# Kernel tuning notes

Hardware: AMD Instinct MI355X
Metric: run time of the kernel (lower is better)

The kernel has to match this reference:

```python
import jax, jax.numpy as jnp
import numpy as np

EMBED = 1024
HEADS = 16
HEAD_DIM = EMBED // HEADS
MAX_REL = 8
B, S = 4, 1024


def setup_inputs() -> dict:
    key = jax.random.key(0)
    ks = jax.random.split(key, 12)
    lim = 1.0 / np.sqrt(EMBED)
    def lin(k):
        k1, k2 = jax.random.split(k)
        W = jax.random.uniform(k1, (EMBED, EMBED), jnp.float32, -lim, lim)
        b = jax.random.uniform(k2, (EMBED,), jnp.float32, -lim, lim)
        return W, b
    Wq, bq = lin(ks[0]); Wk, bk = lin(ks[1]); Wv, bv = lin(ks[2]); Wo, bo = lin(ks[3])
    return {
        'query': jax.random.normal(ks[4], (B, S, EMBED), jnp.float32),
        'key': jax.random.normal(ks[5], (B, S, EMBED), jnp.float32),
        'value': jax.random.normal(ks[6], (B, S, EMBED), jnp.float32),
        'mask': jnp.zeros((B, S, S), dtype=bool),
        'Wq': Wq, 'bq': bq, 'Wk': Wk, 'bk': bk, 'Wv': Wv, 'bv': bv,
        'Wo': Wo, 'bo': bo,
        'rel_bias': jnp.zeros((HEADS, 2 * MAX_REL + 1), jnp.float32),
    }


def _split_heads(x):
    b, s, _ = x.shape
    return x.reshape(b, s, HEADS, HEAD_DIM).transpose(0, 2, 1, 3)  # [b,h,s,d]


def reference(query, key, value, mask, Wq, bq, Wk, bk, Wv, bv, Wo, bo, rel_bias):
    scale = jnp.sqrt(jnp.float32(HEAD_DIM))
    Q = _split_heads(query @ Wq.T + bq)
    K = _split_heads(key @ Wk.T + bk)
    V = _split_heads(value @ Wv.T + bv)
    scores = jnp.einsum('bhqd,bhkd->bhqk', Q, K) / scale
    # relative position bias: rel_bias[h, clip(j-i)+max]
    idx = jnp.arange(query.shape[1])
    rel = jnp.clip(idx[None, :] - idx[:, None], -MAX_REL, MAX_REL) + MAX_REL  # [s,s]
    bias = rel_bias[:, rel]  # [h,s,s]
    scores = scores + bias[None]
    scores = jnp.where(mask[:, None, :, :], -jnp.inf, scores)
    attn = jax.nn.softmax(scores, axis=-1)
    ctx = jnp.einsum('bhqk,bhkd->bhqd', attn, V)
    b, h, s, d = ctx.shape
    out = ctx.transpose(0, 2, 1, 3).reshape(b, s, h * d) @ Wo.T + bo
    return out, attn, scores
```

## Files before the change

kernel.cpp:

```cpp
#include <hip/hip_runtime.h>

typedef __bf16 bf16_t;
typedef bf16_t bf16x4 __attribute__((ext_vector_type(4)));
typedef bf16_t bf16x8 __attribute__((ext_vector_type(8)));
typedef float f32x4 __attribute__((ext_vector_type(4)));
typedef float f32x8 __attribute__((ext_vector_type(8)));

#define B_N 4
#define S_N 1024
#define E_N 1024
#define H_N 16
#define D_N 64

#define MFMA16 __builtin_amdgcn_mfma_f32_16x16x32_bf16

static __device__ __forceinline__ bf16_t f2b(float x) { return (bf16_t)x; }

static __device__ __forceinline__ void gload_lds16(const void* g, void* l) {
  __builtin_amdgcn_global_load_lds(
      (const __attribute__((address_space(1))) unsigned int*)g,
      (__attribute__((address_space(3))) unsigned int*)l, 16, 0, 0);
}

static __device__ __forceinline__ void lds_barrier() {
  asm volatile("s_waitcnt lgkmcnt(0)\n\ts_barrier" ::: "memory");
  __builtin_amdgcn_sched_barrier(0);
}

__global__ __launch_bounds__(256) void convert_kernel(
    const float* __restrict__ q, const float* __restrict__ k, const float* __restrict__ v,
    const float* __restrict__ wq, const float* __restrict__ wk,
    const float* __restrict__ wv, const float* __restrict__ wo,
    bf16_t* __restrict__ dq, bf16_t* __restrict__ dk, bf16_t* __restrict__ dv,
    bf16_t* __restrict__ dwq, bf16_t* __restrict__ dwk,
    bf16_t* __restrict__ dwv, bf16_t* __restrict__ dwo)
{
  const size_t e = ((size_t)blockIdx.x * 256 + threadIdx.x) * 8;
  const float* src; bf16_t* dst; size_t off;
  if (e < 12582912ull) {
    const int which = (int)(e >> 22);
    off = e & 4194303ull;
    src = which == 0 ? q : (which == 1 ? k : v);
    dst = which == 0 ? dq : (which == 1 ? dk : dv);
  } else {
    const size_t e2 = e - 12582912ull;
    const int which = (int)(e2 >> 20);
    off = e2 & 1048575ull;
    src = which == 0 ? wq : (which == 1 ? wk : (which == 2 ? wv : wo));
    dst = which == 0 ? dwq : (which == 1 ? dwk : (which == 2 ? dwv : dwo));
  }
  f32x8 x = *(const f32x8*)(src + off);
  bf16x8 r;
#pragma unroll
  for (int i = 0; i < 8; ++i) r[i] = f2b(x[i]);
  *(bf16x8*)(dst + off) = r;
}

__global__ __launch_bounds__(256) void mask_rowany(
    const unsigned char* __restrict__ mask, unsigned char* __restrict__ flags)
{
  const int row = blockIdx.x * 4 + (threadIdx.x >> 6);
  const int lane = threadIdx.x & 63;
  const uint4 v = *(const uint4*)(mask + (size_t)row * 1024 + lane * 16);
  const unsigned int any = v.x | v.y | v.z | v.w;
  const unsigned long long bal = __ballot(any != 0);
  if (lane == 0) flags[row] = bal ? 1 : 0;
}

__global__ __launch_bounds__(256) void qkv_gemm(
    const bf16_t* __restrict__ qA, const bf16_t* __restrict__ kA, const bf16_t* __restrict__ vA,
    const bf16_t* __restrict__ Wq, const bf16_t* __restrict__ Wk, const bf16_t* __restrict__ Wv,
    const float* __restrict__ bq, const float* __restrict__ bk, const float* __restrict__ bv,
    bf16_t* __restrict__ Qo, bf16_t* __restrict__ Ko, bf16_t* __restrict__ Vto)
{
  const int z = blockIdx.z;
  const bf16_t* A = z == 0 ? qA : (z == 1 ? kA : vA);
  const bf16_t* W = z == 0 ? Wq : (z == 1 ? Wk : Wv);
  const float* bias = z == 0 ? bq : (z == 1 ? bk : bv);

  __shared__ bf16_t As[128 * 32];
  __shared__ bf16_t Bs[128 * 32];
  const int tid = threadIdx.x;
  const int m0 = blockIdx.y * 128, n0 = blockIdx.x * 128;
  const int lane = tid & 63, wid = tid >> 6;
  const int wr = wid >> 1, wc = wid & 1;
  const int lr = lane & 15, lh = lane >> 4;
  const int sr = lane >> 2, sc = (lane & 3) * 8;
  f32x4 acc[4][4] = {};
  for (int k0 = 0; k0 < 1024; k0 += 32) {
#pragma unroll
    for (int i = 0; i < 2; ++i) {
      const int br = wid * 32 + i * 16;
      gload_lds16(&A[(size_t)(m0 + br + sr) * 1024 + k0 + sc], &As[br * 32]);
      gload_lds16(&W[(size_t)(n0 + br + sr) * 1024 + k0 + sc], &Bs[br * 32]);
    }
    __syncthreads();
    bf16x8 af[4], bw[4];
#pragma unroll
    for (int m = 0; m < 4; ++m)
      af[m] = *(const bf16x8*)&As[(wr * 64 + m * 16 + lr) * 32 + lh * 8];
#pragma unroll
    for (int n = 0; n < 4; ++n)
      bw[n] = *(const bf16x8*)&Bs[(wc * 64 + n * 16 + lr) * 32 + lh * 8];
#pragma unroll
    for (int m = 0; m < 4; ++m)
#pragma unroll
      for (int n = 0; n < 4; ++n)
        acc[m][n] = MFMA16(af[m], bw[n], acc[m][n], 0, 0, 0);
    __syncthreads();
  }
#pragma unroll
  for (int n = 0; n < 4; ++n) {
    const int col = n0 + wc * 64 + n * 16 + lr;
    const float bv_ = bias[col];
    const int h = col >> 6, d = col & 63;
#pragma unroll
    for (int m = 0; m < 4; ++m) {
      const int row0 = m0 + wr * 64 + m * 16 + lh * 4;
#pragma unroll
      for (int r = 0; r < 4; ++r) {
        const int row = row0 + r;
        const float v = acc[m][n][r] + bv_;
        const int b = row >> 10, s = row & 1023;
        if (z == 0)
          Qo[((size_t)(b * H_N + h) * S_N + s) * D_N + d] = f2b(v);
        else if (z == 1)
          Ko[((size_t)(b * H_N + h) * S_N + s) * D_N + d] = f2b(v);
        else
          Vto[((size_t)(b * H_N + h) * D_N + d) * S_N + s] = f2b(v);
      }
    }
  }
}

__global__ __launch_bounds__(256) void out_gemm(
    const bf16_t* __restrict__ A, const bf16_t* __restrict__ W,
    const float* __restrict__ bias, float* __restrict__ Co)
{
  __shared__ bf16_t As[128 * 32];
  __shared__ bf16_t Bs[128 * 32];
  const int tid = threadIdx.x;
  const int m0 = blockIdx.y * 128, n0 = blockIdx.x * 128;
  const int lane = tid & 63, wid = tid >> 6;
  const int wr = wid >> 1, wc = wid & 1;
  const int lr = lane & 15, lh = lane >> 4;
  const int sr = lane >> 2, sc = (lane & 3) * 8;
  f32x4 acc[4][4] = {};
  for (int k0 = 0; k0 < 1024; k0 += 32) {
#pragma unroll
    for (int i = 0; i < 2; ++i) {
      const int br = wid * 32 + i * 16;
      gload_lds16(&A[(size_t)(m0 + br + sr) * 1024 + k0 + sc], &As[br * 32]);
      gload_lds16(&W[(size_t)(n0 + br + sr) * 1024 + k0 + sc], &Bs[br * 32]);
    }
    __syncthreads();
    bf16x8 af[4], bw[4];
#pragma unroll
    for (int m = 0; m < 4; ++m)
      af[m] = *(const bf16x8*)&As[(wr * 64 + m * 16 + lr) * 32 + lh * 8];
#pragma unroll
    for (int n = 0; n < 4; ++n)
      bw[n] = *(const bf16x8*)&Bs[(wc * 64 + n * 16 + lr) * 32 + lh * 8];
#pragma unroll
    for (int m = 0; m < 4; ++m)
#pragma unroll
      for (int n = 0; n < 4; ++n)
        acc[m][n] = MFMA16(af[m], bw[n], acc[m][n], 0, 0, 0);
    __syncthreads();
  }
#pragma unroll
  for (int n = 0; n < 4; ++n) {
    const int col = n0 + wc * 64 + n * 16 + lr;
    const float bv_ = bias[col];
#pragma unroll
    for (int m = 0; m < 4; ++m) {
      const int row0 = m0 + wr * 64 + m * 16 + lh * 4;
#pragma unroll
      for (int r = 0; r < 4; ++r)
        Co[(size_t)(row0 + r) * E_N + col] = acc[m][n][r] + bv_;
    }
  }
}

static __device__ __forceinline__ f32x4 score4(
    f32x4 acc, int qrow, int kc, const unsigned char* __restrict__ mrow,
    const float* __restrict__ rbh, float rb_lo, float rb_hi, bool um)
{
  const int d0 = kc - qrow;
  float b0, b1, b2, b3;
  if (d0 >= 8) { b0 = b1 = b2 = b3 = rb_hi; }
  else if (d0 <= -11) { b0 = b1 = b2 = b3 = rb_lo; }
  else {
    int dd;
    dd = d0;     dd = dd < -8 ? -8 : (dd > 8 ? 8 : dd); b0 = rbh[dd + 8];
    dd = d0 + 1; dd = dd < -8 ? -8 : (dd > 8 ? 8 : dd); b1 = rbh[dd + 8];
    dd = d0 + 2; dd = dd < -8 ? -8 : (dd > 8 ? 8 : dd); b2 = rbh[dd + 8];
    dd = d0 + 3; dd = dd < -8 ? -8 : (dd > 8 ? 8 : dd); b3 = rbh[dd + 8];
  }
  f32x4 s;
  s[0] = acc[0] * 0.125f + b0;
  s[1] = acc[1] * 0.125f + b1;
  s[2] = acc[2] * 0.125f + b2;
  s[3] = acc[3] * 0.125f + b3;
  if (um) {
    const unsigned int mw = *(const unsigned int*)(mrow + kc);
    const float NEG = -__builtin_inff();
    if (mw & 0xffu)       s[0] = NEG;
    if (mw & 0xff00u)     s[1] = NEG;
    if (mw & 0xff0000u)   s[2] = NEG;
    if (mw & 0xff000000u) s[3] = NEG;
  }
  return s;
}

__global__ __launch_bounds__(256) void fused_attn(
    const bf16_t* __restrict__ Q, const bf16_t* __restrict__ K,
    const bf16_t* __restrict__ Vt,
    const unsigned char* __restrict__ mask, const unsigned char* __restrict__ rowflag,
    const float* __restrict__ rel_bias,
    float* __restrict__ scores, float* __restrict__ attn, bf16_t* __restrict__ ctx)
{
  __shared__ bf16_t Ktile[64 * 64];
  __shared__ bf16_t Vtile[64 * 64];
  __shared__ float S_lds[4][16][68];

  const int bh = blockIdx.y, b = bh >> 4, h = bh & 15;
  const int q0 = blockIdx.x * 64;
  const int tid = threadIdx.x;
  const int w = tid >> 6, lane = tid & 63;
  const int lr = lane & 15, lh = lane >> 4;
  const int qrow = q0 + w * 16 + lr;

  const bf16_t* Qh = Q + (size_t)bh * (S_N * D_N);
  const bf16_t* Kh = K + (size_t)bh * (S_N * D_N);
  const bf16_t* Vh = Vt + (size_t)bh * (D_N * S_N);
  const unsigned char* mrow = mask + (size_t)b * S_N * S_N + (size_t)qrow * S_N;
  float* Sbase = scores + (size_t)bh * S_N * S_N + (size_t)(q0 + w * 16) * S_N;
  float* Abase = attn + (size_t)bh * S_N * S_N + (size_t)(q0 + w * 16) * S_N;
  const float* rbh = rel_bias + h * 17;
  const float rb_lo = rbh[0], rb_hi = rbh[16];
  const float NEG = -__builtin_inff();
  const float THR = 8.0f;
  const bool um = rowflag[b * S_N + qrow] != 0;

  const int sg_row0 = tid >> 3, sg_c = tid & 7;
  const int sg_row1 = (tid + 256) >> 3;
  const int sg_s0 = (sg_c ^ (sg_row0 & 7)) * 8;
  const int sg_s1 = (sg_c ^ (sg_row1 & 7)) * 8;

  bf16x8 qa0 = *(const bf16x8*)&Qh[(size_t)qrow * D_N + lh * 8];
  bf16x8 qa1 = *(const bf16x8*)&Qh[(size_t)qrow * D_N + 32 + lh * 8];

  const int ks0 = (lh ^ (lr & 7)) * 8;
  const int ks1 = ((4 + lh) ^ (lr & 7)) * 8;

  float mrun = NEG, srun = 0.f;
  for (int kt = 0; kt < 16; ++kt) {
    const int kb = kt * 64;
    lds_barrier();
    *(bf16x8*)&Ktile[sg_row0 * 64 + sg_s0] =
        *(const bf16x8*)&Kh[(size_t)(kb + sg_row0) * D_N + sg_c * 8];
    *(bf16x8*)&Ktile[sg_row1 * 64 + sg_s1] =
        *(const bf16x8*)&Kh[(size_t)(kb + sg_row1) * D_N + sg_c * 8];
    lds_barrier();
    f32x4 sr4[4];
    float mloc = NEG;
#pragma unroll
    for (int t = 0; t < 4; ++t) {
      const int krow = t * 16 + lr;
      bf16x8 ka0 = *(const bf16x8*)&Ktile[krow * 64 + ks0];
      bf16x8 ka1 = *(const bf16x8*)&Ktile[krow * 64 + ks1];
      f32x4 acc = {};
      acc = MFMA16(ka0, qa0, acc, 0, 0, 0);
      acc = MFMA16(ka1, qa1, acc, 0, 0, 0);
      const int kc = kb + t * 16 + 4 * lh;
      f32x4 s = score4(acc, qrow, kc, mrow, rbh, rb_lo, rb_hi, um);
      sr4[t] = s;
      *(f32x4*)&S_lds[w][lr][t * 16 + 4 * lh] = s;
      mloc = fmaxf(mloc, fmaxf(fmaxf(s[0], s[1]), fmaxf(s[2], s[3])));
    }
    mloc = fmaxf(mloc, __shfl_xor(mloc, 16));
    mloc = fmaxf(mloc, __shfl_xor(mloc, 32));
    if (__any(mloc - mrun > THR)) {
      const float mn = fmaxf(mrun, mloc);
      if (mn > NEG) {
        srun = srun * __expf(mrun - mn);
        mrun = mn;
      }
    }
    const bool live = mrun > NEG;
    float ls = 0.f;
#pragma unroll
    for (int t = 0; t < 4; ++t) {
      f32x4 s = sr4[t];
      float e0 = live ? __expf(s[0] - mrun) : 0.f;
      float e1 = live ? __expf(s[1] - mrun) : 0.f;
      float e2 = live ? __expf(s[2] - mrun) : 0.f;
      float e3 = live ? __expf(s[3] - mrun) : 0.f;
      ls += (e0 + e1) + (e2 + e3);
    }
    srun += ls;
#pragma unroll
    for (int i = 0; i < 4; ++i) {
      const int row = 4 * i + lh;
      f32x4 sv = *(const f32x4*)&S_lds[w][row][lr * 4];
      __builtin_nontemporal_store(sv, (f32x4*)&Sbase[(size_t)row * S_N + kb + lr * 4]);
    }
  }
  srun += __shfl_xor(srun, 16);
  srun += __shfl_xor(srun, 32);
  const float M = mrun;
  const float invs = 1.0f / srun;

  f32x4 accp[4] = {};
  for (int kt = 0; kt < 16; ++kt) {
    const int kb = kt * 64;
    lds_barrier();
    *(bf16x8*)&Ktile[sg_row0 * 64 + sg_s0] =
        *(const bf16x8*)&Kh[(size_t)(kb + sg_row0) * D_N + sg_c * 8];
    *(bf16x8*)&Ktile[sg_row1 * 64 + sg_s1] =
        *(const bf16x8*)&Kh[(size_t)(kb + sg_row1) * D_N + sg_c * 8];
    *(bf16x8*)&Vtile[sg_row0 * 64 + sg_s0] =
        *(const bf16x8*)&Vh[(size_t)sg_row0 * S_N + kb + sg_c * 8];
    *(bf16x8*)&Vtile[sg_row1 * 64 + sg_s1] =
        *(const bf16x8*)&Vh[(size_t)sg_row1 * S_N + kb + sg_c * 8];
    lds_barrier();
#pragma unroll
    for (int t = 0; t < 4; ++t) {
      const int krow = t * 16 + lr;
      bf16x8 ka0 = *(const bf16x8*)&Ktile[krow * 64 + ks0];
      bf16x8 ka1 = *(const bf16x8*)&Ktile[krow * 64 + ks1];
      f32x4 acc = {};
      acc = MFMA16(ka0, qa0, acc, 0, 0, 0);
      acc = MFMA16(ka1, qa1, acc, 0, 0, 0);
      const int kc = kb + t * 16 + 4 * lh;
      f32x4 s = score4(acc, qrow, kc, mrow, rbh, rb_lo, rb_hi, um);
      f32x4 p;
#pragma unroll
      for (int j = 0; j < 4; ++j) p[j] = __expf(s[j] - M) * invs;
      *(f32x4*)&S_lds[w][lr][t * 16 + 4 * lh] = p;
    }
#pragma unroll
    for (int i = 0; i < 4; ++i) {
      const int row = 4 * i + lh;
      f32x4 pv = *(const f32x4*)&S_lds[w][row][lr * 4];
      __builtin_nontemporal_store(pv, (f32x4*)&Abase[(size_t)row * S_N + kb + lr * 4]);
    }
#pragma unroll
    for (int ch = 0; ch < 2; ++ch) {
      f32x8 pf = *(const f32x8*)&S_lds[w][lr][ch * 32 + lh * 8];
      bf16x8 pa;
#pragma unroll
      for (int j = 0; j < 8; ++j) pa[j] = f2b(pf[j]);
#pragma unroll
      for (int dt = 0; dt < 4; ++dt) {
        const int drow = dt * 16 + lr;
        bf16x8 vb = *(const bf16x8*)&Vtile[drow * 64 + (((ch * 4 + lh) ^ (lr & 7)) * 8)];
        accp[dt] = MFMA16(pa, vb, accp[dt], 0, 0, 0);
      }
    }
  }
#pragma unroll
  for (int dt = 0; dt < 4; ++dt)
#pragma unroll
    for (int r = 0; r < 4; ++r)
      ctx[((size_t)(b * S_N + q0 + w * 16 + 4 * lh + r)) * E_N + h * 64 + dt * 16 + lr] =
          f2b(accp[dt][r]);
}

extern "C" void kernel_launch(void* const* d_in, const int* in_sizes, int n_in,
                              void* d_out, int out_size, void* d_ws, size_t ws_size,
                              hipStream_t stream) {
  (void)in_sizes; (void)n_in; (void)out_size; (void)ws_size;
  const float* query = (const float*)d_in[0];
  const float* key   = (const float*)d_in[1];
  const float* value = (const float*)d_in[2];
  const unsigned char* mask = (const unsigned char*)d_in[3];
  const float* Wq = (const float*)d_in[4];
  const float* bq = (const float*)d_in[5];
  const float* Wk = (const float*)d_in[6];
  const float* bk = (const float*)d_in[7];
  const float* Wv = (const float*)d_in[8];
  const float* bv = (const float*)d_in[9];
  const float* Wo = (const float*)d_in[10];
  const float* bo = (const float*)d_in[11];
  const float* rel_bias = (const float*)d_in[12];

  float* out_f    = (float*)d_out;
  float* attn_f   = out_f + (size_t)4194304;
  float* scores_f = attn_f + (size_t)67108864;

  char* ws = (char*)d_ws;
  bf16_t* qbf  = (bf16_t*)(ws);
  bf16_t* kbf  = (bf16_t*)(ws + (8ull  << 20));
  bf16_t* vbf  = (bf16_t*)(ws + (16ull << 20));
  bf16_t* Wqb  = (bf16_t*)(ws + (24ull << 20));
  bf16_t* Wkb  = (bf16_t*)(ws + (26ull << 20));
  bf16_t* Wvb  = (bf16_t*)(ws + (28ull << 20));
  bf16_t* Wob  = (bf16_t*)(ws + (30ull << 20));
  bf16_t* Qbf  = (bf16_t*)(ws + (32ull << 20));
  bf16_t* Kbf  = (bf16_t*)(ws + (40ull << 20));
  bf16_t* Vtbf = (bf16_t*)(ws + (48ull << 20));
  bf16_t* CTX  = (bf16_t*)(ws + (56ull << 20));
  unsigned char* FLAGS = (unsigned char*)(ws + (64ull << 20));

  convert_kernel<<<dim3(8192), dim3(256), 0, stream>>>(
      query, key, value, Wq, Wk, Wv, Wo, qbf, kbf, vbf, Wqb, Wkb, Wvb, Wob);
  mask_rowany<<<dim3(1024), dim3(256), 0, stream>>>(mask, FLAGS);
  qkv_gemm<<<dim3(8, 32, 3), dim3(256), 0, stream>>>(
      qbf, kbf, vbf, Wqb, Wkb, Wvb, bq, bk, bv, Qbf, Kbf, Vtbf);
  fused_attn<<<dim3(16, 64), dim3(256), 0, stream>>>(
      Qbf, Kbf, Vtbf, mask, FLAGS, rel_bias, scores_f, attn_f, CTX);
  out_gemm<<<dim3(8, 32), dim3(256), 0, stream>>>(CTX, Wob, bo, out_f);
}
```

Baseline: 223.0 us.

## Merge mask scan into convert, shrink out_gemm tiles, prefetch K/V tiles in attention

Folds the mask row-any kernel into the conversion kernel as extra blocks, removing one launch. The output GEMM tile shrinks from 128x128 to 64x128, doubling the grid from 256 to 512 blocks so more CUs are busy, at the cost of less operand reuse per block. In the fused attention kernel, K and V tiles for the next iteration are loaded into registers while the current tile is in use, to hide global load latency. This raises register pressure.

```diff
diff --git a/kernel.cpp b/kernel.cpp
--- a/kernel.cpp
+++ b/kernel.cpp
@@ -27,14 +27,24 @@
   __builtin_amdgcn_sched_barrier(0);
 }
 
-__global__ __launch_bounds__(256) void convert_kernel(
+__global__ __launch_bounds__(256) void convert_mask_kernel(
     const float* __restrict__ q, const float* __restrict__ k, const float* __restrict__ v,
     const float* __restrict__ wq, const float* __restrict__ wk,
     const float* __restrict__ wv, const float* __restrict__ wo,
     bf16_t* __restrict__ dq, bf16_t* __restrict__ dk, bf16_t* __restrict__ dv,
     bf16_t* __restrict__ dwq, bf16_t* __restrict__ dwk,
-    bf16_t* __restrict__ dwv, bf16_t* __restrict__ dwo)
+    bf16_t* __restrict__ dwv, bf16_t* __restrict__ dwo,
+    const unsigned char* __restrict__ mask, unsigned char* __restrict__ flags)
 {
+  if (blockIdx.x >= 8192) {
+    const int row = (blockIdx.x - 8192) * 4 + (threadIdx.x >> 6);
+    const int lane = threadIdx.x & 63;
+    const uint4 mv = *(const uint4*)(mask + (size_t)row * 1024 + lane * 16);
+    const unsigned int any = mv.x | mv.y | mv.z | mv.w;
+    const unsigned long long bal = __ballot(any != 0);
+    if (lane == 0) flags[row] = bal ? 1 : 0;
+    return;
+  }
   const size_t e = ((size_t)blockIdx.x * 256 + threadIdx.x) * 8;
   const float* src; bf16_t* dst; size_t off;
   if (e < 12582912ull) {
@@ -56,17 +66,6 @@
   *(bf16x8*)(dst + off) = r;
 }
 
-__global__ __launch_bounds__(256) void mask_rowany(
-    const unsigned char* __restrict__ mask, unsigned char* __restrict__ flags)
-{
-  const int row = blockIdx.x * 4 + (threadIdx.x >> 6);
-  const int lane = threadIdx.x & 63;
-  const uint4 v = *(const uint4*)(mask + (size_t)row * 1024 + lane * 16);
-  const unsigned int any = v.x | v.y | v.z | v.w;
-  const unsigned long long bal = __ballot(any != 0);
-  if (lane == 0) flags[row] = bal ? 1 : 0;
-}
-
 __global__ __launch_bounds__(256) void qkv_gemm(
     const bf16_t* __restrict__ qA, const bf16_t* __restrict__ kA, const bf16_t* __restrict__ vA,
     const bf16_t* __restrict__ Wq, const bf16_t* __restrict__ Wk, const bf16_t* __restrict__ Wv,
@@ -137,44 +136,43 @@
     const bf16_t* __restrict__ A, const bf16_t* __restrict__ W,
     const float* __restrict__ bias, float* __restrict__ Co)
 {
-  __shared__ bf16_t As[128 * 32];
+  __shared__ bf16_t As[64 * 32];
   __shared__ bf16_t Bs[128 * 32];
   const int tid = threadIdx.x;
-  const int m0 = blockIdx.y * 128, n0 = blockIdx.x * 128;
+  const int m0 = blockIdx.y * 64, n0 = blockIdx.x * 128;
   const int lane = tid & 63, wid = tid >> 6;
-  const int wr = wid >> 1, wc = wid & 1;
   const int lr = lane & 15, lh = lane >> 4;
   const int sr = lane >> 2, sc = (lane & 3) * 8;
-  f32x4 acc[4][4] = {};
+  f32x4 acc[4][2] = {};
   for (int k0 = 0; k0 < 1024; k0 += 32) {
+    gload_lds16(&A[(size_t)(m0 + wid * 16 + sr) * 1024 + k0 + sc], &As[wid * 16 * 32]);
 #pragma unroll
     for (int i = 0; i < 2; ++i) {
       const int br = wid * 32 + i * 16;
-      gload_lds16(&A[(size_t)(m0 + br + sr) * 1024 + k0 + sc], &As[br * 32]);
       gload_lds16(&W[(size_t)(n0 + br + sr) * 1024 + k0 + sc], &Bs[br * 32]);
     }
     __syncthreads();
-    bf16x8 af[4], bw[4];
+    bf16x8 af[4], bw[2];
 #pragma unroll
     for (int m = 0; m < 4; ++m)
-      af[m] = *(const bf16x8*)&As[(wr * 64 + m * 16 + lr) * 32 + lh * 8];
-#pragma unroll
-    for (int n = 0; n < 4; ++n)
-      bw[n] = *(const bf16x8*)&Bs[(wc * 64 + n * 16 + lr) * 32 + lh * 8];
+      af[m] = *(const bf16x8*)&As[(m * 16 + lr) * 32 + lh * 8];
+#pragma unroll
+    for (int n = 0; n < 2; ++n)
+      bw[n] = *(const bf16x8*)&Bs[(wid * 32 + n * 16 + lr) * 32 + lh * 8];
 #pragma unroll
     for (int m = 0; m < 4; ++m)
 #pragma unroll
-      for (int n = 0; n < 4; ++n)
+      for (int n = 0; n < 2; ++n)
         acc[m][n] = MFMA16(af[m], bw[n], acc[m][n], 0, 0, 0);
     __syncthreads();
   }
 #pragma unroll
-  for (int n = 0; n < 4; ++n) {
-    const int col = n0 + wc * 64 + n * 16 + lr;
+  for (int n = 0; n < 2; ++n) {
+    const int col = n0 + wid * 32 + n * 16 + lr;
     const float bv_ = bias[col];
 #pragma unroll
     for (int m = 0; m < 4; ++m) {
-      const int row0 = m0 + wr * 64 + m * 16 + lh * 4;
+      const int row0 = m0 + m * 16 + lh * 4;
 #pragma unroll
       for (int r = 0; r < 4; ++r)
         Co[(size_t)(row0 + r) * E_N + col] = acc[m][n][r] + bv_;
@@ -244,7 +242,7 @@
   const bool um = rowflag[b * S_N + qrow] != 0;
 
   const int sg_row0 = tid >> 3, sg_c = tid & 7;
-  const int sg_row1 = (tid + 256) >> 3;
+  const int sg_row1 = sg_row0 + 32;
   const int sg_s0 = (sg_c ^ (sg_row0 & 7)) * 8;
   const int sg_s1 = (sg_c ^ (sg_row1 & 7)) * 8;
 
@@ -255,13 +253,18 @@
   const int ks1 = ((4 + lh) ^ (lr & 7)) * 8;
 
   float mrun = NEG, srun = 0.f;
+  bf16x8 krA = *(const bf16x8*)&Kh[(size_t)sg_row0 * D_N + sg_c * 8];
+  bf16x8 krB = *(const bf16x8*)&Kh[(size_t)sg_row1 * D_N + sg_c * 8];
   for (int kt = 0; kt < 16; ++kt) {
     const int kb = kt * 64;
     lds_barrier();
-    *(bf16x8*)&Ktile[sg_row0 * 64 + sg_s0] =
-        *(const bf16x8*)&Kh[(size_t)(kb + sg_row0) * D_N + sg_c * 8];
-    *(bf16x8*)&Ktile[sg_row1 * 64 + sg_s1] =
-        *(const bf16x8*)&Kh[(size_t)(kb + sg_row1) * D_N + sg_c * 8];
+    *(bf16x8*)&Ktile[sg_row0 * 64 + sg_s0] = krA;
+    *(bf16x8*)&Ktile[sg_row1 * 64 + sg_s1] = krB;
+    if (kt + 1 < 16) {
+      const int kn = kb + 64;
+      krA = *(const bf16x8*)&Kh[(size_t)(kn + sg_row0) * D_N + sg_c * 8];
+      krB = *(const bf16x8*)&Kh[(size_t)(kn + sg_row1) * D_N + sg_c * 8];
+    }
     lds_barrier();
     f32x4 sr4[4];
     float mloc = NEG;
@@ -313,17 +316,24 @@
   const float invs = 1.0f / srun;
 
   f32x4 accp[4] = {};
+  krA = *(const bf16x8*)&Kh[(size_t)sg_row0 * D_N + sg_c * 8];
+  krB = *(const bf16x8*)&Kh[(size_t)sg_row1 * D_N + sg_c * 8];
+  bf16x8 vrA = *(const bf16x8*)&Vh[(size_t)sg_row0 * S_N + sg_c * 8];
+  bf16x8 vrB = *(const bf16x8*)&Vh[(size_t)sg_row1 * S_N + sg_c * 8];
   for (int kt = 0; kt < 16; ++kt) {
     const int kb = kt * 64;
     lds_barrier();
-    *(bf16x8*)&Ktile[sg_row0 * 64 + sg_s0] =
-        *(const bf16x8*)&Kh[(size_t)(kb + sg_row0) * D_N + sg_c * 8];
-    *(bf16x8*)&Ktile[sg_row1 * 64 + sg_s1] =
-        *(const bf16x8*)&Kh[(size_t)(kb + sg_row1) * D_N + sg_c * 8];
-    *(bf16x8*)&Vtile[sg_row0 * 64 + sg_s0] =
-        *(const bf16x8*)&Vh[(size_t)sg_row0 * S_N + kb + sg_c * 8];
-    *(bf16x8*)&Vtile[sg_row1 * 64 + sg_s1] =
-        *(const bf16x8*)&Vh[(size_t)sg_row1 * S_N + kb + sg_c * 8];
+    *(bf16x8*)&Ktile[sg_row0 * 64 + sg_s0] = krA;
+    *(bf16x8*)&Ktile[sg_row1 * 64 + sg_s1] = krB;
+    *(bf16x8*)&Vtile[sg_row0 * 64 + sg_s0] = vrA;
+    *(bf16x8*)&Vtile[sg_row1 * 64 + sg_s1] = vrB;
+    if (kt + 1 < 16) {
+      const int kn = kb + 64;
+      krA = *(const bf16x8*)&Kh[(size_t)(kn + sg_row0) * D_N + sg_c * 8];
+      krB = *(const bf16x8*)&Kh[(size_t)(kn + sg_row1) * D_N + sg_c * 8];
+      vrA = *(const bf16x8*)&Vh[(size_t)sg_row0 * S_N + kn + sg_c * 8];
+      vrB = *(const bf16x8*)&Vh[(size_t)sg_row1 * S_N + kn + sg_c * 8];
+    }
     lds_barrier();
 #pragma unroll
     for (int t = 0; t < 4; ++t) {
@@ -404,12 +414,12 @@
   bf16_t* CTX  = (bf16_t*)(ws + (56ull << 20));
   unsigned char* FLAGS = (unsigned char*)(ws + (64ull << 20));
 
-  convert_kernel<<<dim3(8192), dim3(256), 0, stream>>>(
-      query, key, value, Wq, Wk, Wv, Wo, qbf, kbf, vbf, Wqb, Wkb, Wvb, Wob);
-  mask_rowany<<<dim3(1024), dim3(256), 0, stream>>>(mask, FLAGS);
+  convert_mask_kernel<<<dim3(9216), dim3(256), 0, stream>>>(
+      query, key, value, Wq, Wk, Wv, Wo, qbf, kbf, vbf, Wqb, Wkb, Wvb, Wob,
+      mask, FLAGS);
   qkv_gemm<<<dim3(8, 32, 3), dim3(256), 0, stream>>>(
       qbf, kbf, vbf, Wqb, Wkb, Wvb, bq, bk, bv, Qbf, Kbf, Vtbf);
   fused_attn<<<dim3(16, 64), dim3(256), 0, stream>>>(
       Qbf, Kbf, Vtbf, mask, FLAGS, rel_bias, scores_f, attn_f, CTX);
-  out_gemm<<<dim3(8, 32), dim3(256), 0, stream>>>(CTX, Wob, bo, out_f);
-}
+  out_gemm<<<dim3(8, 64), dim3(256), 0, stream>>>(CTX, Wob, bo, out_f);
+}
```

After: 228.0 us. +2.2%, slower.
